# Performance work log

Measured on AMD Instinct MI355X. Metric: run time of the kernel, lower is better.

## Reference

```python
import jax, jax.numpy as jnp
import numpy as np

# e2m1 nibble -> float LUT (indices 0..7 positive, 8..15 negative), per mxfp4 spec
E2M1_LUT = jnp.array([0.0, 0.5, 1.0, 1.5, 2.0, 3.0, 4.0, 6.0,
                      -0.0, -0.5, -1.0, -1.5, -2.0, -3.0, -4.0, -6.0], dtype=jnp.float32)


def mxfp4_dequant(scales, blocks):
    """scales: [E, R, K//32] int (uint8 values); blocks: [E, R, K//32, 16] int (uint8 values).
    Returns dequantized weight [E, K, R] (transposed like the original)."""
    low = blocks & 15
    high = (blocks >> 4) & 15
    interleaved = jnp.stack([low, high], axis=-1)            # [E, R, K//32, 16, 2]
    interleaved = interleaved.reshape(blocks.shape[:-1] + (32,))  # [E, R, K//32, 32]
    vals = E2M1_LUT[interleaved]                             # [E, R, K//32, 32] f32
    exp = scales.astype(jnp.int32) - 127                     # biased uint8 exponent
    deq = jnp.ldexp(vals, exp[..., None])                    # scale each block
    deq = deq.reshape(deq.shape[:-2] + (-1,))                # [E, R, K]
    return deq.transpose(0, 2, 1)                            # [E, K, R]


def rmsnorm(x, w, eps=1e-5):
    var = jnp.mean(x * x, axis=-1, keepdims=True)
    return x * jax.lax.rsqrt(var + eps) * w


def setup_inputs() -> dict:
    key = jax.random.key(0)
    ks = jax.random.split(key, 8)
    T, H, D, E = 1024, 2048, 2048, 8
    return {
        "x": jax.random.normal(ks[0], (T, H), dtype=jnp.float32),
        "norm_weight": jnp.ones((H,), dtype=jnp.float32),
        "router_weight": jax.random.normal(ks[1], (H, E), dtype=jnp.float32) * 0.02,
        "router_bias": jnp.zeros((E,), dtype=jnp.float32),
        "gate_up_scales": jax.random.randint(ks[2], (E, 2 * D, H // 32), 0, 132, dtype=jnp.int32),
        "gate_up_blocks": jax.random.randint(ks[3], (E, 2 * D, H // 32, 16), 0, 256, dtype=jnp.int32),
        "gate_up_bias": jax.random.normal(ks[4], (E, 2 * D), dtype=jnp.float32) * 0.02,
        "down_scales": jax.random.randint(ks[5], (E, H, D // 32), 0, 132, dtype=jnp.int32),
        "down_blocks": jax.random.randint(ks[6], (E, H, D // 32, 16), 0, 256, dtype=jnp.int32),
        "down_bias": jax.random.normal(ks[7], (E, H), dtype=jnp.float32) * 0.02,
        "k": 4,
    }


def reference(x, norm_weight, router_weight, router_bias,
              gate_up_scales, gate_up_blocks, gate_up_bias,
              down_scales, down_blocks, down_bias, k):
    alpha, limit = 1.702, 7.0
    W_gu = mxfp4_dequant(gate_up_scales, gate_up_blocks)   # [E, H, 2D]
    W_down = mxfp4_dequant(down_scales, down_blocks)       # [E, D, H]

    t = rmsnorm(x, norm_weight)                            # [T, H]
    logits = t @ router_weight + router_bias               # [T, E]
    top_v, top_i = jax.lax.top_k(logits, k)                # [T, k]
    top_v = jax.nn.softmax(top_v, axis=-1)
    tok = jnp.arange(logits.shape[0])[:, None]             # [T, 1]
    scores = jnp.zeros_like(logits).at[tok, top_i].set(top_v)  # [T, E]

    # dense all-expert compute, masked post-hoc by router scores (as in original)
    gate_up = jnp.einsum('th,ehd->etd', t, W_gu) + gate_up_bias[:, None, :]  # [E, T, 2D]
    gate = jnp.minimum(gate_up[..., ::2], limit)
    up = jnp.clip(gate_up[..., 1::2], -limit, limit)
    glu = gate * jax.nn.sigmoid(gate * alpha)
    nxt = jnp.einsum('etd,edh->eth', (up + 1.0) * glu, W_down) + down_bias[:, None, :]  # [E, T, H]
    nxt = nxt * scores.T[..., None]                        # weight by router scores
    return jnp.sum(nxt, axis=0) + x
```

## Files before the change

### kernel.cpp

```cpp
#include <hip/hip_runtime.h>
#include <hip/hip_bf16.h>
#include <stdint.h>

#define T_TOK 1024
#define HDIM 2048
#define DDIM 2048
#define NE 8

typedef unsigned int uint;
typedef unsigned short ushort;

typedef _Float16 f16x8 __attribute__((ext_vector_type(8)));
typedef float f32x4 __attribute__((ext_vector_type(4)));

typedef __attribute__((address_space(1))) const void v_g;
typedef __attribute__((address_space(3))) void v_l;

__device__ __forceinline__ ushort f2h(float f) {
  _Float16 h = (_Float16)f;
  return *(ushort*)&h;
}

__device__ __forceinline__ uint dqh(uint nib, int sc) {
  uint m = nib & 7u;
  int e = (int)(m >> 1);
  int e16 = sc - 113 + e;
  uint mant = ((m & 1u) && m >= 2u) ? 0x200u : 0u;
  uint bits;
  if (m == 0u || e16 <= -10) bits = 0u;
  else if (e16 >= 1) bits = ((uint)e16 << 10) | mant;
  else bits = (0x400u | mant) >> (1 - e16);
  return bits | ((nib & 8u) << 12);
}
__device__ __forceinline__ uint dq2h(uint b, int sc) {
  return dqh(b & 15u, sc) | (dqh((b >> 4) & 15u, sc) << 16);
}

__device__ __forceinline__ void dq_block(
    const int* __restrict__ qb, const int* __restrict__ qs,
    ushort* __restrict__ dst, size_t bi)
{
  int sc = qs[bi];
  const int4* bp = (const int4*)(qb + bi * 16);
  int4 q0 = bp[0], q1 = bp[1], q2 = bp[2], q3 = bp[3];
  uint w[16];
  w[0]=dq2h(q0.x,sc);  w[1]=dq2h(q0.y,sc);  w[2]=dq2h(q0.z,sc);  w[3]=dq2h(q0.w,sc);
  w[4]=dq2h(q1.x,sc);  w[5]=dq2h(q1.y,sc);  w[6]=dq2h(q1.z,sc);  w[7]=dq2h(q1.w,sc);
  w[8]=dq2h(q2.x,sc);  w[9]=dq2h(q2.y,sc);  w[10]=dq2h(q2.z,sc); w[11]=dq2h(q2.w,sc);
  w[12]=dq2h(q3.x,sc); w[13]=dq2h(q3.y,sc); w[14]=dq2h(q3.z,sc); w[15]=dq2h(q3.w,sc);
  uint4* o = (uint4*)(dst + bi * 32);
  o[0] = make_uint4(w[0], w[1], w[2], w[3]);
  o[1] = make_uint4(w[4], w[5], w[6], w[7]);
  o[2] = make_uint4(w[8], w[9], w[10], w[11]);
  o[3] = make_uint4(w[12], w[13], w[14], w[15]);
}

__device__ __forceinline__ void waitv4() {
  asm volatile("s_waitcnt vmcnt(4)" ::: "memory");
  __builtin_amdgcn_sched_barrier(0);
}
__device__ __forceinline__ void waitv0() {
  asm volatile("s_waitcnt vmcnt(0)" ::: "memory");
  __builtin_amdgcn_sched_barrier(0);
}
__device__ __forceinline__ void barrier_raw() {
  asm volatile("" ::: "memory");
  __builtin_amdgcn_s_barrier();
  asm volatile("" ::: "memory");
}

__device__ __forceinline__ void router_body(
    int t, const float* __restrict__ x, const float* __restrict__ nw,
    const float* __restrict__ rw, const float* __restrict__ rb,
    ushort* __restrict__ tbuf, float* __restrict__ scores)
{
  const int tid = threadIdx.x;
  const float4* xr = (const float4*)(x + (size_t)t * HDIM);
  float4 v0 = xr[tid * 2], v1 = xr[tid * 2 + 1];
  float ss = v0.x*v0.x + v0.y*v0.y + v0.z*v0.z + v0.w*v0.w
           + v1.x*v1.x + v1.y*v1.y + v1.z*v1.z + v1.w*v1.w;
  __shared__ float red[256];
  red[tid] = ss;
  __syncthreads();
  for (int s = 128; s > 0; s >>= 1) {
    if (tid < s) red[tid] += red[tid + s];
    __syncthreads();
  }
  const float rstd = rsqrtf(red[0] * (1.0f / HDIM) + 1e-5f);
  float xv[8] = {v0.x, v0.y, v0.z, v0.w, v1.x, v1.y, v1.z, v1.w};
  float lp[NE];
#pragma unroll
  for (int e = 0; e < NE; ++e) lp[e] = 0.f;
  union { ushort us[8]; uint4 v; } pkh;
  const int h0 = tid * 8;
#pragma unroll
  for (int j = 0; j < 8; ++j) {
    int h = h0 + j;
    float tn = xv[j] * rstd * nw[h];
    pkh.us[j] = f2h(tn);
#pragma unroll
    for (int e = 0; e < NE; ++e) lp[e] += tn * rw[h * NE + e];
  }
  *(uint4*)(tbuf + (size_t)t * HDIM + h0) = pkh.v;
#pragma unroll
  for (int e = 0; e < NE; ++e)
#pragma unroll
    for (int off = 32; off > 0; off >>= 1) lp[e] += __shfl_down(lp[e], off);
  __shared__ float wred[4][NE];
  if ((tid & 63) == 0) {
#pragma unroll
    for (int e = 0; e < NE; ++e) wred[tid >> 6][e] = lp[e];
  }
  __syncthreads();
  if (tid == 0) {
    float lg[NE];
#pragma unroll
    for (int e = 0; e < NE; ++e)
      lg[e] = wred[0][e] + wred[1][e] + wred[2][e] + wred[3][e] + rb[e];
    bool used[NE] = {false, false, false, false, false, false, false, false};
    float tv[4]; int ti[4];
    for (int s = 0; s < 4; ++s) {
      float best = -3.4e38f; int bi = 0;
      for (int e = 0; e < NE; ++e)
        if (!used[e] && lg[e] > best) { best = lg[e]; bi = e; }
      used[bi] = true; tv[s] = best; ti[s] = bi;
    }
    float den = 0.f, ev[4];
    for (int s = 0; s < 4; ++s) { ev[s] = expf(tv[s] - tv[0]); den += ev[s]; }
    float so[NE] = {0, 0, 0, 0, 0, 0, 0, 0};
    for (int s = 0; s < 4; ++s) so[ti[s]] = ev[s] / den;
#pragma unroll
    for (int e = 0; e < NE; ++e) scores[t * NE + e] = so[e];
  }
}

__global__ __launch_bounds__(256) void router_kernel(
    const float* __restrict__ x, const float* __restrict__ nw,
    const float* __restrict__ rw, const float* __restrict__ rb,
    ushort* __restrict__ tbuf, float* __restrict__ scores)
{
  router_body(blockIdx.x, x, nw, rw, rb, tbuf, scores);
}

#define NGUB (NE * 4096 * 64 / 256)
__global__ __launch_bounds__(256) void prep_kernel(
    const float* __restrict__ x, const float* __restrict__ nw,
    const float* __restrict__ rw, const float* __restrict__ rb,
    const int* __restrict__ gub, const int* __restrict__ gus,
    ushort* __restrict__ tbuf, float* __restrict__ scores,
    ushort* __restrict__ wgu)
{
  if (blockIdx.x >= NGUB) {
    router_body(blockIdx.x - NGUB, x, nw, rw, rb, tbuf, scores);
    return;
  }
  size_t bi = (size_t)blockIdx.x * 256 + threadIdx.x;
  dq_block(gub, gus, wgu, bi);
}

__global__ __launch_bounds__(256) void scan_kernel(
    const float* __restrict__ scores, int* __restrict__ cnts,
    int* __restrict__ idx, int* __restrict__ slotmap)
{
  const int e = blockIdx.x, tid = threadIdx.x;
  int loc[4], c = 0;
#pragma unroll
  for (int j = 0; j < 4; ++j) {
    int t = tid * 4 + j;
    loc[j] = (scores[t * NE + e] != 0.f) ? 1 : 0;
    c += loc[j];
  }
  __shared__ int sc[256];
  sc[tid] = c;
  __syncthreads();
  for (int off = 1; off < 256; off <<= 1) {
    int v = (tid >= off) ? sc[tid - off] : 0;
    __syncthreads();
    sc[tid] += v;
    __syncthreads();
  }
  int base = sc[tid] - c;
#pragma unroll
  for (int j = 0; j < 4; ++j)
    if (loc[j]) {
      int t = tid * 4 + j;
      idx[e * T_TOK + base] = t;
      slotmap[t * NE + e] = base;
      base++;
    }
  if (tid == 255) cnts[e] = sc[255];
}

template<int MODE>
__global__ __launch_bounds__(256) void mx_gemm_p(
    const ushort* __restrict__ Abase,
    const ushort* __restrict__ Bw,
    const float* __restrict__ bias,
    const float* __restrict__ scores,
    const int* __restrict__ cnts,
    const int* __restrict__ tokidx,
    ushort* __restrict__ midH,
    float* __restrict__ outp,
    const int* __restrict__ dnb,
    const int* __restrict__ dns,
    ushort* __restrict__ wdn)
{
  constexpr int NTOT = (MODE == 0) ? 2 * DDIM : HDIM;
  constexpr int K    = (MODE == 0) ? HDIM : DDIM;
  constexpr int NKT  = K / 32;
  const int nt = blockIdx.x, mt = blockIdx.y, e = blockIdx.z;
  if constexpr (MODE == 0) {
    if (e >= NE) {
      size_t bi = ((size_t)(e - NE) * 256 + mt * 32 + nt) * 256 + threadIdx.x;
      dq_block(dnb, dns, wdn, bi);
      return;
    }
  }
  const int cnt = cnts[e];
  const int m0 = mt * 128, n0 = nt * 128;
  if (m0 >= cnt) return;
  const ushort* A = Abase + (MODE == 0 ? (size_t)0 : (size_t)e * T_TOK * DDIM);

  __shared__ __align__(16) ushort As[2][128 * 32];
  __shared__ __align__(16) ushort Bs[2][128 * 32];
  __shared__ int tok_s[128];

  const int tid = threadIdx.x;
  const int lane = tid & 63;
  const int wv = tid >> 6;
  const int wm = wv >> 1, wn = wv & 1;
  const int fr = lane & 15, kg = lane >> 4;

  if (tid < 128) {
    int sl = m0 + tid;
    tok_s[tid] = (sl < cnt) ? tokidx[e * T_TOK + sl] : 0;
  }
  __syncthreads();

  int arow[2];
#pragma unroll
  for (int j = 0; j < 2; ++j) {
    int row = (tid + 256 * j) >> 2;
    arow[j] = (MODE == 0) ? tok_s[row] : (m0 + row);
  }

  f32x4 acc[4][4];
#pragma unroll
  for (int i = 0; i < 4; ++i)
#pragma unroll
    for (int j = 0; j < 4; ++j) acc[i][j] = f32x4{0.f, 0.f, 0.f, 0.f};

  auto do_stage = [&](int buf, int kt) {
#pragma unroll
    for (int j = 0; j < 2; ++j) {
      int cidx = tid + 256 * j;
      int row = cidx >> 2, ck = cidx & 3;
      int gck = ck ^ ((row >> 1) & 3);
      size_t go = (size_t)arow[j] * K + kt * 32 + gck * 8;
      __builtin_amdgcn_global_load_lds((v_g*)(A + go),
          (v_l*)((char*)&As[buf][0] + cidx * 16), 16, 0, 0);
    }
#pragma unroll
    for (int j = 0; j < 2; ++j) {
      int cidx = tid + 256 * j;
      int row = cidx >> 2, ck = cidx & 3;
      int gck = ck ^ ((row >> 1) & 3);
      const ushort* g = Bw + ((size_t)e * NTOT + n0 + row) * K + kt * 32 + gck * 8;
      __builtin_amdgcn_global_load_lds((v_g*)g,
          (v_l*)((char*)&Bs[buf][0] + cidx * 16), 16, 0, 0);
    }
  };

  auto do_compute = [&](int buf) {
    f16x8 aF[4], bF[4];
#pragma unroll
    for (int mi = 0; mi < 4; ++mi) {
      int r = wm * 64 + mi * 16 + fr;
      int ck = kg ^ ((r >> 1) & 3);
      aF[mi] = *(const f16x8*)(&As[buf][r * 32 + ck * 8]);
    }
#pragma unroll
    for (int ni = 0; ni < 4; ++ni) {
      int r = wn * 64 + ni * 16 + fr;
      int ck = kg ^ ((r >> 1) & 3);
      bF[ni] = *(const f16x8*)(&Bs[buf][r * 32 + ck * 8]);
    }
#pragma unroll
    for (int mi = 0; mi < 4; ++mi)
#pragma unroll
      for (int ni = 0; ni < 4; ++ni)
        acc[mi][ni] = __builtin_amdgcn_mfma_f32_16x16x32_f16(aF[mi], bF[ni], acc[mi][ni], 0, 0, 0);
  };

  do_stage(0, 0);
  do_stage(1, 1);
  waitv4();
  barrier_raw();
#pragma unroll 2
  for (int kt = 0; kt < NKT; ++kt) {
    do_compute(kt & 1);
    if (kt == NKT - 1) break;
    barrier_raw();
    if (kt + 2 < NKT) {
      do_stage(kt & 1, kt + 2);
      waitv4();
    } else {
      waitv0();
    }
    barrier_raw();
  }

  const int c = lane & 15, rg = lane >> 4;
  const int sbase = m0 + wm * 64, nbase = n0 + wn * 64;
  if constexpr (MODE == 0) {
#pragma unroll
    for (int mi = 0; mi < 4; ++mi)
#pragma unroll
      for (int ni = 0; ni < 4; ++ni) {
        int n = nbase + ni * 16 + c;
        float bv = bias[(size_t)e * NTOT + n];
#pragma unroll
        for (int r = 0; r < 4; ++r) {
          int slot = sbase + mi * 16 + rg * 4 + r;
          float val = acc[mi][ni][r] + bv;
          float other = __shfl_xor(val, 1);
          if (!(c & 1) && slot < cnt) {
            int tok = tok_s[slot - m0];
            float g = fminf(val, 7.0f);
            float u = fminf(fmaxf(other, -7.0f), 7.0f);
            float glu = g / (1.0f + expf(-1.702f * g));
            float mv = (u + 1.0f) * glu;
            float s = scores[tok * NE + e];
            midH[((size_t)e * T_TOK + slot) * DDIM + ((uint)n >> 1)] = f2h(mv * s);
          }
        }
      }
  } else if constexpr (MODE == 1) {
#pragma unroll
    for (int mi = 0; mi < 4; ++mi)
#pragma unroll
      for (int ni = 0; ni < 4; ++ni) {
        int n = nbase + ni * 16 + c;
        float dbv = bias[(size_t)e * NTOT + n];
#pragma unroll
        for (int r = 0; r < 4; ++r) {
          int slot = sbase + mi * 16 + rg * 4 + r;
          if (slot < cnt) {
            int tok = tok_s[slot - m0];
            float s = scores[tok * NE + e];
            atomicAdd(outp + (size_t)tok * HDIM + n, acc[mi][ni][r] + s * dbv);
          }
        }
      }
  } else {
#pragma unroll
    for (int mi = 0; mi < 4; ++mi)
#pragma unroll
      for (int ni = 0; ni < 4; ++ni) {
        int n = nbase + ni * 16 + c;
#pragma unroll
        for (int r = 0; r < 4; ++r) {
          int slot = sbase + mi * 16 + rg * 4 + r;
          if (slot < cnt)
            midH[((size_t)e * T_TOK + slot) * HDIM + n] = f2h(acc[mi][ni][r]);
        }
      }
  }
}

__global__ __launch_bounds__(256) void gather_kernel(
    const float* __restrict__ x, const ushort* __restrict__ midD,
    const float* __restrict__ dnbias, const float* __restrict__ scores,
    const int* __restrict__ slotmap, float* __restrict__ outp)
{
  const int t = blockIdx.x, tid = threadIdx.x;
  const int h0 = tid * 8;
  const float4* xr = (const float4*)(x + (size_t)t * HDIM + h0);
  float4 a0 = xr[0], a1 = xr[1];
  float sc[NE]; int sl[NE];
#pragma unroll
  for (int e = 0; e < NE; ++e) sc[e] = scores[t * NE + e];
#pragma unroll
  for (int e = 0; e < NE; ++e) sl[e] = slotmap[t * NE + e];
#pragma unroll
  for (int e = 0; e < NE; ++e) {
    if (sc[e] != 0.f) {
      const f16x8 m8 = *(const f16x8*)(midD + ((size_t)e * T_TOK + sl[e]) * HDIM + h0);
      const float4* br = (const float4*)(dnbias + (size_t)e * HDIM + h0);
      float4 b0 = br[0], b1 = br[1];
      float s = sc[e];
      a0.x += (float)m8[0] + s * b0.x; a0.y += (float)m8[1] + s * b0.y;
      a0.z += (float)m8[2] + s * b0.z; a0.w += (float)m8[3] + s * b0.w;
      a1.x += (float)m8[4] + s * b1.x; a1.y += (float)m8[5] + s * b1.y;
      a1.z += (float)m8[6] + s * b1.z; a1.w += (float)m8[7] + s * b1.w;
    }
  }
  float4* orow = (float4*)(outp + (size_t)t * HDIM + h0);
  orow[0] = a0;
  orow[1] = a1;
}

__global__ __launch_bounds__(256) void gu_gemm_q(
    const ushort* __restrict__ At,
    const int* __restrict__ qblocks,
    const int* __restrict__ qscales,
    const float* __restrict__ bias,
    const float* __restrict__ scores,
    const int* __restrict__ cnts,
    const int* __restrict__ tokidx,
    ushort* __restrict__ midH)
{
  constexpr int NTOT = 2 * DDIM;
  constexpr int K = HDIM;
  const int nt = blockIdx.x, mt = blockIdx.y, e = blockIdx.z;
  const int cnt = cnts[e];
  const int m0 = mt * 128, n0 = nt * 128;
  if (m0 >= cnt) return;

  __shared__ __align__(16) ushort As[128 * 64];
  __shared__ __align__(16) ushort Bs[128 * 64];
  __shared__ int tok_s[128];

  const int tid = threadIdx.x;
  const int lane = tid & 63;
  const int wv = tid >> 6;
  const int wm = wv >> 1, wn = wv & 1;
  const int fr = lane & 15, kg = lane >> 4;

  if (tid < 128) {
    int sl = m0 + tid;
    tok_s[tid] = (sl < cnt) ? tokidx[e * T_TOK + sl] : 0;
  }
  __syncthreads();
  int arow[4];
#pragma unroll
  for (int j = 0; j < 4; ++j) arow[j] = tok_s[(tid + 256 * j) >> 3];

  f32x4 acc[4][4];
#pragma unroll
  for (int i = 0; i < 4; ++i)
#pragma unroll
    for (int j = 0; j < 4; ++j) acc[i][j] = f32x4{0.f, 0.f, 0.f, 0.f};

  for (int kt = 0; kt < K / 64; ++kt) {
#pragma unroll
    for (int j = 0; j < 4; ++j) {
      int cidx = tid + 256 * j;
      int row = cidx >> 3, ck = cidx & 7;
      int sck = ck ^ (row & 7);
      size_t go = (size_t)arow[j] * K + kt * 64 + sck * 8;
      __builtin_amdgcn_global_load_lds((v_g*)(At + go), (v_l*)((char*)As + cidx * 16), 16, 0, 0);
    }
    {
      const int brow = tid >> 1, bblk = tid & 1;
      int kb = kt * 2 + bblk;
      size_t bi = ((size_t)e * NTOT + n0 + brow) * (K / 32) + kb;
      int sc = qscales[bi];
      const int4* bp = (const int4*)(qblocks + bi * 16);
      int4 q0 = bp[0], q1 = bp[1], q2 = bp[2], q3 = bp[3];
      uint w[16];
      w[0]=dq2h(q0.x,sc);  w[1]=dq2h(q0.y,sc);  w[2]=dq2h(q0.z,sc);  w[3]=dq2h(q0.w,sc);
      w[4]=dq2h(q1.x,sc);  w[5]=dq2h(q1.y,sc);  w[6]=dq2h(q1.z,sc);  w[7]=dq2h(q1.w,sc);
      w[8]=dq2h(q2.x,sc);  w[9]=dq2h(q2.y,sc);  w[10]=dq2h(q2.z,sc); w[11]=dq2h(q2.w,sc);
      w[12]=dq2h(q3.x,sc); w[13]=dq2h(q3.y,sc); w[14]=dq2h(q3.z,sc); w[15]=dq2h(q3.w,sc);
#pragma unroll
      for (int q = 0; q < 4; ++q) {
        int ck = bblk * 4 + q;
        int sk = ck ^ (brow & 7);
        *(uint4*)((char*)Bs + brow * 128 + sk * 16) =
            make_uint4(w[4*q], w[4*q+1], w[4*q+2], w[4*q+3]);
      }
    }
    __syncthreads();
#pragma unroll
    for (int kh = 0; kh < 2; ++kh) {
      f16x8 aF[4], bF[4];
#pragma unroll
      for (int mi = 0; mi < 4; ++mi) {
        int r = wm * 64 + mi * 16 + fr;
        int ck = (kh * 4 + kg) ^ (r & 7);
        aF[mi] = *(const f16x8*)((const char*)As + r * 128 + ck * 16);
      }
#pragma unroll
      for (int ni = 0; ni < 4; ++ni) {
        int r = wn * 64 + ni * 16 + fr;
        int ck = (kh * 4 + kg) ^ (r & 7);
        bF[ni] = *(const f16x8*)((const char*)Bs + r * 128 + ck * 16);
      }
#pragma unroll
      for (int mi = 0; mi < 4; ++mi)
#pragma unroll
        for (int ni = 0; ni < 4; ++ni)
          acc[mi][ni] = __builtin_amdgcn_mfma_f32_16x16x32_f16(aF[mi], bF[ni], acc[mi][ni], 0, 0, 0);
    }
    __syncthreads();
  }

  const int c = lane & 15, rg = lane >> 4;
  const int sbase = m0 + wm * 64, nbase = n0 + wn * 64;
#pragma unroll
  for (int mi = 0; mi < 4; ++mi)
#pragma unroll
    for (int ni = 0; ni < 4; ++ni) {
      int n = nbase + ni * 16 + c;
      float bv = bias[(size_t)e * NTOT + n];
#pragma unroll
      for (int r = 0; r < 4; ++r) {
        int slot = sbase + mi * 16 + rg * 4 + r;
        float val = acc[mi][ni][r] + bv;
        float other = __shfl_xor(val, 1);
        if (!(c & 1) && slot < cnt) {
          int tok = tok_s[slot - m0];
          float g = fminf(val, 7.0f);
          float u = fminf(fmaxf(other, -7.0f), 7.0f);
          float glu = g / (1.0f + expf(-1.702f * g));
          float mv = (u + 1.0f) * glu;
          float s = scores[tok * NE + e];
          midH[((size_t)e * T_TOK + slot) * DDIM + ((uint)n >> 1)] = f2h(mv * s);
        }
      }
    }
}

__global__ __launch_bounds__(256) void dn_gemm_q(
    const ushort* __restrict__ Abase,
    const int* __restrict__ qblocks,
    const int* __restrict__ qscales,
    const float* __restrict__ bias,
    const float* __restrict__ scores,
    const int* __restrict__ cnts,
    const int* __restrict__ tokidx,
    float* __restrict__ outp)
{
  constexpr int NTOT = HDIM;
  constexpr int K    = DDIM;
  const int nt = blockIdx.x, mt = blockIdx.y, e = blockIdx.z;
  const int cnt = cnts[e];
  const int m0 = mt * 128, n0 = nt * 128;
  if (m0 >= cnt) return;
  const ushort* A = Abase + (size_t)e * T_TOK * DDIM;

  __shared__ __align__(16) ushort As[128 * 64];
  __shared__ __align__(16) ushort Bs[128 * 64];
  __shared__ int tok_s[128];

  const int tid = threadIdx.x;
  const int lane = tid & 63;
  const int wv = tid >> 6;
  const int wm = wv >> 1, wn = wv & 1;
  const int fr = lane & 15, kg = lane >> 4;

  if (tid < 128) {
    int sl = m0 + tid;
    tok_s[tid] = (sl < cnt) ? tokidx[e * T_TOK + sl] : 0;
  }
  __syncthreads();

  f32x4 acc[4][4];
#pragma unroll
  for (int i = 0; i < 4; ++i)
#pragma unroll
    for (int j = 0; j < 4; ++j) acc[i][j] = f32x4{0.f, 0.f, 0.f, 0.f};

  for (int kt = 0; kt < K / 64; ++kt) {
#pragma unroll
    for (int j = 0; j < 4; ++j) {
      int cidx = tid + 256 * j;
      int row = cidx >> 3, ck = cidx & 7;
      int sck = ck ^ (row & 7);
      size_t go = (size_t)(m0 + row) * K + kt * 64 + sck * 8;
      __builtin_amdgcn_global_load_lds((v_g*)(A + go), (v_l*)((char*)As + cidx * 16), 16, 0, 0);
    }
    {
      const int brow = tid >> 1, bblk = tid & 1;
      int kb = kt * 2 + bblk;
      size_t bi = ((size_t)e * NTOT + n0 + brow) * (K / 32) + kb;
      int sc = qscales[bi];
      const int4* bp = (const int4*)(qblocks + bi * 16);
      int4 q0 = bp[0], q1 = bp[1], q2 = bp[2], q3 = bp[3];
      uint w[16];
      w[0]=dq2h(q0.x,sc);  w[1]=dq2h(q0.y,sc);  w[2]=dq2h(q0.z,sc);  w[3]=dq2h(q0.w,sc);
      w[4]=dq2h(q1.x,sc);  w[5]=dq2h(q1.y,sc);  w[6]=dq2h(q1.z,sc);  w[7]=dq2h(q1.w,sc);
      w[8]=dq2h(q2.x,sc);  w[9]=dq2h(q2.y,sc);  w[10]=dq2h(q2.z,sc); w[11]=dq2h(q2.w,sc);
      w[12]=dq2h(q3.x,sc); w[13]=dq2h(q3.y,sc); w[14]=dq2h(q3.z,sc); w[15]=dq2h(q3.w,sc);
#pragma unroll
      for (int q = 0; q < 4; ++q) {
        int ck = bblk * 4 + q;
        int sk = ck ^ (brow & 7);
        *(uint4*)((char*)Bs + brow * 128 + sk * 16) =
            make_uint4(w[4*q], w[4*q+1], w[4*q+2], w[4*q+3]);
      }
    }
    __syncthreads();
#pragma unroll
    for (int kh = 0; kh < 2; ++kh) {
      f16x8 aF[4], bF[4];
#pragma unroll
      for (int mi = 0; mi < 4; ++mi) {
        int r = wm * 64 + mi * 16 + fr;
        int ck = (kh * 4 + kg) ^ (r & 7);
        aF[mi] = *(const f16x8*)((const char*)As + r * 128 + ck * 16);
      }
#pragma unroll
      for (int ni = 0; ni < 4; ++ni) {
        int r = wn * 64 + ni * 16 + fr;
        int ck = (kh * 4 + kg) ^ (r & 7);
        bF[ni] = *(const f16x8*)((const char*)Bs + r * 128 + ck * 16);
      }
#pragma unroll
      for (int mi = 0; mi < 4; ++mi)
#pragma unroll
        for (int ni = 0; ni < 4; ++ni)
          acc[mi][ni] = __builtin_amdgcn_mfma_f32_16x16x32_f16(aF[mi], bF[ni], acc[mi][ni], 0, 0, 0);
    }
    __syncthreads();
  }

  const int c = lane & 15, rg = lane >> 4;
  const int sbase = m0 + wm * 64, nbase = n0 + wn * 64;
#pragma unroll
  for (int mi = 0; mi < 4; ++mi)
#pragma unroll
    for (int ni = 0; ni < 4; ++ni) {
      int n = nbase + ni * 16 + c;
      float dbv = bias[(size_t)e * NTOT + n];
#pragma unroll
      for (int r = 0; r < 4; ++r) {
        int slot = sbase + mi * 16 + rg * 4 + r;
        if (slot < cnt) {
          int tok = tok_s[slot - m0];
          float s = scores[tok * NE + e];
          atomicAdd(outp + (size_t)tok * HDIM + n, acc[mi][ni][r] + s * dbv);
        }
      }
    }
}

extern "C" void kernel_launch(void* const* d_in, const int* in_sizes, int n_in,
                              void* d_out, int out_size, void* d_ws, size_t ws_size,
                              hipStream_t stream)
{
  const float* x      = (const float*)d_in[0];
  const float* nw     = (const float*)d_in[1];
  const float* rw     = (const float*)d_in[2];
  const float* rb     = (const float*)d_in[3];
  const int*   gus    = (const int*)d_in[4];
  const int*   gub    = (const int*)d_in[5];
  const float* gubias = (const float*)d_in[6];
  const int*   dns    = (const int*)d_in[7];
  const int*   dnb    = (const int*)d_in[8];
  const float* dnbias = (const float*)d_in[9];

  char* ws = (char*)d_ws;
  const size_t SZ_WGU  = (size_t)NE * 4096 * 2048 * 2;
  const size_t SZ_WDN  = (size_t)NE * 2048 * 2048 * 2;
  const size_t SZ_T    = (size_t)T_TOK * HDIM * 2;
  const size_t SZ_MID  = (size_t)NE * T_TOK * DDIM * 2;
  const size_t SZ_MIDD = (size_t)NE * T_TOK * HDIM * 2;
  const size_t SZ_SC   = (size_t)T_TOK * NE * 4;
  const size_t SZ_IDX  = (size_t)NE * T_TOK * 4;
  const size_t SZ_SLOT = (size_t)T_TOK * NE * 4;
  const size_t SZ_CNT  = 128;

  const size_t need_mid = SZ_WGU + SZ_WDN + SZ_T + SZ_MID + SZ_SC + SZ_IDX + SZ_SLOT + SZ_CNT;
  const size_t need_big = need_mid + SZ_MIDD;
  const bool predeq = ws_size >= need_mid;
  const bool bigws  = ws_size >= need_big;

  ushort* wgu = (ushort*)ws;
  ushort* wdn = (ushort*)(ws + SZ_WGU);
  char* base2 = predeq ? (ws + SZ_WGU + SZ_WDN) : ws;
  ushort* tbuf   = (ushort*)base2;
  ushort* midHp  = (ushort*)(base2 + SZ_T);
  float*  scores = (float*)(base2 + SZ_T + SZ_MID);
  int*    cnts   = (int*)(base2 + SZ_T + SZ_MID + SZ_SC);
  int*    tokidx = (int*)(base2 + SZ_T + SZ_MID + SZ_SC + SZ_CNT);
  int*    slotmap= (int*)(base2 + SZ_T + SZ_MID + SZ_SC + SZ_CNT + SZ_IDX);
  ushort* midD   = (ushort*)(base2 + SZ_T + SZ_MID + SZ_SC + SZ_CNT + SZ_IDX + SZ_SLOT);
  float*  outp   = (float*)d_out;

  if (predeq) {
    prep_kernel<<<NGUB + T_TOK, 256, 0, stream>>>(
        x, nw, rw, rb, gub, gus, tbuf, scores, wgu);
    scan_kernel<<<NE, 256, 0, stream>>>(scores, cnts, tokidx, slotmap);
    mx_gemm_p<0><<<dim3(32, 8, NE + 16), 256, 0, stream>>>(
        tbuf, wgu, gubias, scores, cnts, tokidx, midHp, nullptr, dnb, dns, wdn);
    if (bigws) {
      mx_gemm_p<2><<<dim3(16, 8, NE), 256, 0, stream>>>(
          midHp, wdn, dnbias, scores, cnts, tokidx, midD, nullptr, nullptr, nullptr, nullptr);
      gather_kernel<<<T_TOK, 256, 0, stream>>>(
          x, midD, dnbias, scores, slotmap, outp);
    } else {
      hipMemcpyAsync(d_out, (void*)x, (size_t)T_TOK * HDIM * 4,
                     hipMemcpyDeviceToDevice, stream);
      mx_gemm_p<1><<<dim3(16, 8, NE), 256, 0, stream>>>(
          midHp, wdn, dnbias, scores, cnts, tokidx, nullptr, outp, nullptr, nullptr, nullptr);
    }
  } else {
    hipMemcpyAsync(d_out, (void*)x, (size_t)T_TOK * HDIM * 4,
                   hipMemcpyDeviceToDevice, stream);
    router_kernel<<<T_TOK, 256, 0, stream>>>(x, nw, rw, rb, tbuf, scores);
    scan_kernel<<<NE, 256, 0, stream>>>(scores, cnts, tokidx, slotmap);
    gu_gemm_q<<<dim3(32, 8, NE), 256, 0, stream>>>(
        tbuf, gub, gus, gubias, scores, cnts, tokidx, midHp);
    dn_gemm_q<<<dim3(16, 8, NE), 256, 0, stream>>>(
        midHp, dnb, dns, dnbias, scores, cnts, tokidx, outp);
  }
}
```

Baseline: 289.6 us.

## Split-K the down-projection GEMM in two halves and sum partials in gather

```diff
diff --git a/kernel.cpp b/kernel.cpp
--- a/kernel.cpp
+++ b/kernel.cpp
@@ -207,8 +207,12 @@
 {
   constexpr int NTOT = (MODE == 0) ? 2 * DDIM : HDIM;
   constexpr int K    = (MODE == 0) ? HDIM : DDIM;
-  constexpr int NKT  = K / 32;
-  const int nt = blockIdx.x, mt = blockIdx.y, e = blockIdx.z;
+  constexpr int KSPAN = (MODE == 2) ? K / 2 : K;
+  constexpr int NKT  = KSPAN / 32;
+  const int nt = blockIdx.x, mt = blockIdx.y;
+  const int e  = (MODE == 2) ? (blockIdx.z >> 1) : blockIdx.z;
+  const int kh = (MODE == 2) ? (blockIdx.z & 1) : 0;
+  const int koff = kh * KSPAN;
   if constexpr (MODE == 0) {
     if (e >= NE) {
       size_t bi = ((size_t)(e - NE) * 256 + mt * 32 + nt) * 256 + threadIdx.x;
@@ -256,7 +260,7 @@
       int cidx = tid + 256 * j;
       int row = cidx >> 2, ck = cidx & 3;
       int gck = ck ^ ((row >> 1) & 3);
-      size_t go = (size_t)arow[j] * K + kt * 32 + gck * 8;
+      size_t go = (size_t)arow[j] * K + koff + kt * 32 + gck * 8;
       __builtin_amdgcn_global_load_lds((v_g*)(A + go),
           (v_l*)((char*)&As[buf][0] + cidx * 16), 16, 0, 0);
     }
@@ -265,7 +269,7 @@
       int cidx = tid + 256 * j;
       int row = cidx >> 2, ck = cidx & 3;
       int gck = ck ^ ((row >> 1) & 3);
-      const ushort* g = Bw + ((size_t)e * NTOT + n0 + row) * K + kt * 32 + gck * 8;
+      const ushort* g = Bw + ((size_t)e * NTOT + n0 + row) * K + koff + kt * 32 + gck * 8;
       __builtin_amdgcn_global_load_lds((v_g*)g,
           (v_l*)((char*)&Bs[buf][0] + cidx * 16), 16, 0, 0);
     }
@@ -353,6 +357,7 @@
         }
       }
   } else {
+    ushort* plane = midH + (size_t)kh * NE * T_TOK * HDIM;
 #pragma unroll
     for (int mi = 0; mi < 4; ++mi)
 #pragma unroll
@@ -362,7 +367,7 @@
         for (int r = 0; r < 4; ++r) {
           int slot = sbase + mi * 16 + rg * 4 + r;
           if (slot < cnt)
-            midH[((size_t)e * T_TOK + slot) * HDIM + n] = f2h(acc[mi][ni][r]);
+            plane[((size_t)e * T_TOK + slot) * HDIM + n] = f2h(acc[mi][ni][r]);
         }
       }
   }
@@ -377,6 +382,7 @@
   const int h0 = tid * 8;
   const float4* xr = (const float4*)(x + (size_t)t * HDIM + h0);
   float4 a0 = xr[0], a1 = xr[1];
+  const ushort* midD1 = midD + (size_t)NE * T_TOK * HDIM;
   float sc[NE]; int sl[NE];
 #pragma unroll
   for (int e = 0; e < NE; ++e) sc[e] = scores[t * NE + e];
@@ -385,14 +391,20 @@
 #pragma unroll
   for (int e = 0; e < NE; ++e) {
     if (sc[e] != 0.f) {
-      const f16x8 m8 = *(const f16x8*)(midD + ((size_t)e * T_TOK + sl[e]) * HDIM + h0);
+      size_t off = ((size_t)e * T_TOK + sl[e]) * HDIM + h0;
+      const f16x8 m8 = *(const f16x8*)(midD + off);
+      const f16x8 p8 = *(const f16x8*)(midD1 + off);
       const float4* br = (const float4*)(dnbias + (size_t)e * HDIM + h0);
       float4 b0 = br[0], b1 = br[1];
       float s = sc[e];
-      a0.x += (float)m8[0] + s * b0.x; a0.y += (float)m8[1] + s * b0.y;
-      a0.z += (float)m8[2] + s * b0.z; a0.w += (float)m8[3] + s * b0.w;
-      a1.x += (float)m8[4] + s * b1.x; a1.y += (float)m8[5] + s * b1.y;
-      a1.z += (float)m8[6] + s * b1.z; a1.w += (float)m8[7] + s * b1.w;
+      a0.x += (float)m8[0] + (float)p8[0] + s * b0.x;
+      a0.y += (float)m8[1] + (float)p8[1] + s * b0.y;
+      a0.z += (float)m8[2] + (float)p8[2] + s * b0.z;
+      a0.w += (float)m8[3] + (float)p8[3] + s * b0.w;
+      a1.x += (float)m8[4] + (float)p8[4] + s * b1.x;
+      a1.y += (float)m8[5] + (float)p8[5] + s * b1.y;
+      a1.z += (float)m8[6] + (float)p8[6] + s * b1.z;
+      a1.w += (float)m8[7] + (float)p8[7] + s * b1.w;
     }
   }
   float4* orow = (float4*)(outp + (size_t)t * HDIM + h0);
@@ -656,7 +668,7 @@
   const size_t SZ_WDN  = (size_t)NE * 2048 * 2048 * 2;
   const size_t SZ_T    = (size_t)T_TOK * HDIM * 2;
   const size_t SZ_MID  = (size_t)NE * T_TOK * DDIM * 2;
-  const size_t SZ_MIDD = (size_t)NE * T_TOK * HDIM * 2;
+  const size_t SZ_MIDD = (size_t)2 * NE * T_TOK * HDIM * 2;
   const size_t SZ_SC   = (size_t)T_TOK * NE * 4;
   const size_t SZ_IDX  = (size_t)NE * T_TOK * 4;
   const size_t SZ_SLOT = (size_t)T_TOK * NE * 4;
@@ -686,7 +698,7 @@
     mx_gemm_p<0><<<dim3(32, 8, NE + 16), 256, 0, stream>>>(
         tbuf, wgu, gubias, scores, cnts, tokidx, midHp, nullptr, dnb, dns, wdn);
     if (bigws) {
-      mx_gemm_p<2><<<dim3(16, 8, NE), 256, 0, stream>>>(
+      mx_gemm_p<2><<<dim3(16, 8, NE * 2), 256, 0, stream>>>(
           midHp, wdn, dnbias, scores, cnts, tokidx, midD, nullptr, nullptr, nullptr, nullptr);
       gather_kernel<<<T_TOK, 256, 0, stream>>>(
           x, midD, dnbias, scores, slotmap, outp);
```

Result: no change. 289.4 us, median of 2 (-0.1%).
